# Performance work log

Hardware: AMD Instinct MI355X
Metric: run time of the kernel (lower is better)

The kernel has to match this reference:

```python
import jax, jax.numpy as jnp
import numpy as np

EMBED = 1024
MLP = 2048
N_EXPERTS = 8
TOP_K = 2


def setup_inputs() -> dict:
    key = jax.random.key(0)
    ks = jax.random.split(key, 5)
    scale_e = 1.0 / np.sqrt(EMBED)
    scale_m = 1.0 / np.sqrt(MLP)
    x = jax.random.normal(ks[0], (4, 2048, EMBED), dtype=jnp.float32)
    gate_w = jax.random.normal(ks[1], (EMBED, N_EXPERTS), dtype=jnp.float32) * scale_e
    w1 = jax.random.normal(ks[2], (N_EXPERTS, EMBED, MLP), dtype=jnp.float32) * scale_e
    w3 = jax.random.normal(ks[3], (N_EXPERTS, EMBED, MLP), dtype=jnp.float32) * scale_e
    w2 = jax.random.normal(ks[4], (N_EXPERTS, MLP, EMBED), dtype=jnp.float32) * scale_m
    return {"x": x, "gate_w": gate_w, "w1": w1, "w2": w2, "w3": w3}


def reference(x, gate_w, w1, w2, w3):
    B, S, D = x.shape
    xf = x.reshape(-1, D)  # [T, D] tokens
    # Router: softmax over experts, top-k select, renormalize selected weights
    router_logits = xf @ gate_w                      # [T, E]
    routing_weights = jax.nn.softmax(router_logits, axis=-1)
    sel_w, sel_e = jax.lax.top_k(routing_weights, TOP_K)  # [T, K]
    sel_w = sel_w / jnp.sum(sel_w, axis=-1, keepdims=True)
    out = jnp.zeros_like(xf)
    # Loop over the small fixed expert set; tokens not routed to expert e get
    # coefficient 0, matching the gather/scatter-add combine of the original.
    for e in range(N_EXPERTS):
        coef = jnp.sum(jnp.where(sel_e == e, sel_w, 0.0), axis=-1)  # [T]
        h = jax.nn.silu(xf @ w1[e]) * (xf @ w3[e])                  # [T, Mlp] SwiGLU
        out = out + coef[:, None] * (h @ w2[e])                     # [T, D]
    return out.reshape(B, S, D)
```

## Files before the change

kernel.cpp:

```cpp
#include <hip/hip_runtime.h>

#define EMBED 1024
#define MLP   2048
#define NE    8
#define NTOK  8192
#define RMAX  (2*NTOK + NE*256)

typedef _Float16 f16x8 __attribute__((ext_vector_type(8)));
typedef _Float16 f16x4 __attribute__((ext_vector_type(4)));
typedef float    f32x4 __attribute__((ext_vector_type(4)));

__device__ __forceinline__ void async_copy16(const void* g, void* l) {
  __builtin_amdgcn_global_load_lds(
      (const __attribute__((address_space(1))) unsigned int*)g,
      (__attribute__((address_space(3))) unsigned int*)l, 16, 0, 0);
}

__global__ __launch_bounds__(256) void router_kernel(
    const float* __restrict__ x, const float* __restrict__ gw,
    int* __restrict__ sel_e, float* __restrict__ sel_w, int* __restrict__ counts)
{
  __shared__ float gwt[NE * EMBED];
  __shared__ int cnt[NE];
  int tid = threadIdx.x;
  for (int idx = tid; idx < NE * EMBED; idx += 256) {
    int i = idx >> 3, e = idx & 7;
    gwt[e * EMBED + i] = gw[idx];
  }
  if (tid < NE) cnt[tid] = 0;
  __syncthreads();

  int lane = tid & 63, wv = tid >> 6;
  int t = blockIdx.x * 4 + wv;
  const float4* xr = (const float4*)(x + (size_t)t * EMBED);
  const float4* gt4 = (const float4*)gwt;
  float acc[NE];
  #pragma unroll
  for (int e = 0; e < NE; ++e) acc[e] = 0.f;
  #pragma unroll
  for (int c = 0; c < 4; ++c) {
    float4 xv = xr[c * 64 + lane];
    #pragma unroll
    for (int e = 0; e < NE; ++e) {
      float4 gv = gt4[e * 256 + c * 64 + lane];
      acc[e] += xv.x * gv.x + xv.y * gv.y + xv.z * gv.z + xv.w * gv.w;
    }
  }
  #pragma unroll
  for (int off = 1; off < 64; off <<= 1) {
    #pragma unroll
    for (int e = 0; e < NE; ++e) acc[e] += __shfl_xor(acc[e], off);
  }
  if (lane == 0) {
    int e0 = 0; float l0 = acc[0];
    #pragma unroll
    for (int e = 1; e < NE; ++e) if (acc[e] > l0) { l0 = acc[e]; e0 = e; }
    int e1 = -1; float l1 = -1e30f;
    #pragma unroll
    for (int e = 0; e < NE; ++e) if (e != e0 && acc[e] > l1) { l1 = acc[e]; e1 = e; }
    float w0 = 1.f / (1.f + expf(l1 - l0));
    sel_e[2 * t] = e0;     sel_w[2 * t] = w0;
    sel_e[2 * t + 1] = e1; sel_w[2 * t + 1] = 1.f - w0;
    atomicAdd(&cnt[e0], 1); atomicAdd(&cnt[e1], 1);
  }
  __syncthreads();
  if (tid < NE && cnt[tid]) atomicAdd(&counts[tid], cnt[tid]);
}

__global__ __launch_bounds__(256) void assign_kernel(
    const int* __restrict__ sel_e, const float* __restrict__ sel_w,
    const int* __restrict__ counts, int* __restrict__ cursor,
    int* __restrict__ offs_out, int* __restrict__ rowtok,
    float* __restrict__ rowcoef, int* __restrict__ inv)
{
  int offl[NE];
  {
    int o = 0;
    #pragma unroll
    for (int e = 0; e < NE; ++e) { offl[e] = o; o += (counts[e] + 255) & ~255; }
    if (blockIdx.x == 0 && threadIdx.x == 0) {
      #pragma unroll
      for (int e = 0; e < NE; ++e) offs_out[e] = offl[e];
      offs_out[NE] = o;
    }
  }
  int t = blockIdx.x * 256 + threadIdx.x;
  int lane = threadIdx.x & 63;
  #pragma unroll
  for (int k = 0; k < 2; ++k) {
    int e = sel_e[2 * t + k];
    float w = sel_w[2 * t + k];
    for (int xch = 0; xch < NE; ++xch) {
      unsigned long long m = __ballot(e == xch);
      if (e == xch) {
        int leader = __ffsll((unsigned long long)m) - 1;
        int base = 0;
        if (lane == leader) base = atomicAdd(&cursor[xch], (int)__popcll(m));
        base = __shfl(base, leader);
        int pos = offl[xch] + base + (int)__popcll(m & ((1ull << lane) - 1));
        rowtok[pos] = t;
        rowcoef[pos] = w;
        inv[2 * t + k] = pos;
      }
    }
  }
}

__global__ __launch_bounds__(256) void gather_kernel(
    const float* __restrict__ x, const int* __restrict__ rowtok,
    _Float16* __restrict__ xg)
{
  int r = blockIdx.x;
  int tok = rowtok[r];
  int t4 = threadIdx.x * 4;
  _Float16* dst = xg + (size_t)r * EMBED + t4;
  if (tok >= 0) {
    float4 v = *(const float4*)(x + (size_t)tok * EMBED + t4);
    f16x4 h; h.x = (_Float16)v.x; h.y = (_Float16)v.y; h.z = (_Float16)v.z; h.w = (_Float16)v.w;
    *(f16x4*)dst = h;
  } else {
    f16x4 z = {(_Float16)0.f, (_Float16)0.f, (_Float16)0.f, (_Float16)0.f};
    *(f16x4*)dst = z;
  }
}

__global__ __launch_bounds__(256) void transpose_all_kernel(
    const float* __restrict__ w1, const float* __restrict__ w3,
    const float* __restrict__ w2, _Float16* __restrict__ w1t,
    _Float16* __restrict__ w3t, _Float16* __restrict__ w2t)
{
  int id = blockIdx.x;
  int mat = id >> 12;
  int rr = id & 4095;
  int e = rr >> 9, tile = rr & 511;
  const float* src; _Float16* dst; int K, N;
  if (mat == 0)      { src = w1; dst = w1t; K = EMBED; N = MLP; }
  else if (mat == 1) { src = w3; dst = w3t; K = EMBED; N = MLP; }
  else               { src = w2; dst = w2t; K = MLP;   N = EMBED; }
  int nx = K >> 6;
  int k0 = (tile % nx) * 64, n0 = (tile / nx) * 64;
  src += (size_t)e * K * N;
  dst += (size_t)e * K * N;

  __shared__ float tilebuf[64][65];
  int t = threadIdx.x;
  int r = t >> 4, c4 = (t & 15) * 4;
  #pragma unroll
  for (int i = 0; i < 4; ++i) {
    float4 v = *(const float4*)(src + (size_t)(k0 + r + 16 * i) * N + n0 + c4);
    tilebuf[r + 16 * i][c4 + 0] = v.x;
    tilebuf[r + 16 * i][c4 + 1] = v.y;
    tilebuf[r + 16 * i][c4 + 2] = v.z;
    tilebuf[r + 16 * i][c4 + 3] = v.w;
  }
  __syncthreads();
  int kk8 = (t & 7) * 8, nIdx = t >> 3;
  #pragma unroll
  for (int i = 0; i < 2; ++i) {
    int n = nIdx + 32 * i;
    f16x8 h;
    #pragma unroll
    for (int j = 0; j < 8; ++j) h[j] = (_Float16)tilebuf[kk8 + j][n];
    *(f16x8*)(dst + (size_t)(n0 + n) * K + k0 + kk8) = h;
  }
}

__device__ __forceinline__ int resolve_expert(const int* __restrict__ offs, int r0)
{
  int e = 0;
  #pragma unroll
  for (int q = 0; q < NE - 1; ++q) if (r0 >= offs[q + 1]) e = q + 1;
  return e;
}

__device__ __forceinline__ const _Float16* frag_addr(const _Float16* buf, int row, int quad)
{
  return buf + row * 32 + ((quad ^ ((row >> 1) & 3)) << 3);
}

__global__ __launch_bounds__(512, 2) void gemm1_kernel(
    const _Float16* __restrict__ xg, const _Float16* __restrict__ w1t,
    const _Float16* __restrict__ w3t, const float* __restrict__ rowcoef,
    const int* __restrict__ offs, _Float16* __restrict__ hb)
{
  int r0 = blockIdx.x * 256;
  if (r0 >= offs[NE]) return;
  int e = resolve_expert(offs, r0);
  int n0 = blockIdx.y * 128;
  const _Float16* B1 = w1t + (size_t)e * MLP * EMBED;
  const _Float16* B3 = w3t + (size_t)e * MLP * EMBED;

  __shared__ __align__(16) _Float16 As[2][256 * 32];
  __shared__ __align__(16) _Float16 Bs1[2][128 * 32];
  __shared__ __align__(16) _Float16 Bs3[2][128 * 32];

  int tid = threadIdx.x, lane = tid & 63, wv = tid >> 6;
  int wm = (wv & 3) << 6, wn = (wv >> 2) << 6;
  int l16 = lane & 15, quad = lane >> 4;

  int rowA0 = tid >> 2, kqpA = tid & 3;
  int rowA1 = rowA0 + 128;
  int kqlA0 = kqpA ^ ((rowA0 >> 1) & 3);
  int kqlA1 = kqpA ^ ((rowA1 >> 1) & 3);
  int rowB = tid >> 2, kqpB = tid & 3;
  int kqlB = kqpB ^ ((rowB >> 1) & 3);
  size_t gA0 = (size_t)(r0 + rowA0) * EMBED + kqlA0 * 8;
  size_t gA1 = (size_t)(r0 + rowA1) * EMBED + kqlA1 * 8;
  size_t gB  = (size_t)(n0 + rowB) * EMBED + kqlB * 8;
  int lofA0 = (wv * 64) * 8;
  int lofA1 = (512 + wv * 64) * 8;
  int lofB  = (wv * 64) * 8;

  f32x4 acc1[4][4], acc3[4][4];
  f32x4 z4 = {0.f, 0.f, 0.f, 0.f};
  #pragma unroll
  for (int i = 0; i < 4; ++i)
    #pragma unroll
    for (int j = 0; j < 4; ++j) { acc1[i][j] = z4; acc3[i][j] = z4; }

  auto stage = [&](int b, int kk) {
    async_copy16(xg + gA0 + kk, &As[b][lofA0]);
    async_copy16(xg + gA1 + kk, &As[b][lofA1]);
    async_copy16(B1 + gB  + kk, &Bs1[b][lofB]);
    async_copy16(B3 + gB  + kk, &Bs3[b][lofB]);
  };

  const int NIT = EMBED / 32;
  stage(0, 0);
  for (int k = 0; k < NIT; ++k) {
    int b = k & 1;
    asm volatile("s_waitcnt vmcnt(0)" ::: "memory");
    asm volatile("s_barrier" ::: "memory");
    if (k + 1 < NIT) stage((k + 1) & 1, (k + 1) * 32);

    f16x8 af[4], b1f[4], b3f[4];
    #pragma unroll
    for (int i = 0; i < 4; ++i)
      af[i] = *(const f16x8*)frag_addr(As[b], wm + 16 * i + l16, quad);
    #pragma unroll
    for (int j = 0; j < 4; ++j) {
      b1f[j] = *(const f16x8*)frag_addr(Bs1[b], wn + 16 * j + l16, quad);
      b3f[j] = *(const f16x8*)frag_addr(Bs3[b], wn + 16 * j + l16, quad);
    }
    #pragma unroll
    for (int i = 0; i < 4; ++i)
      #pragma unroll
      for (int j = 0; j < 4; ++j) {
        acc1[i][j] = __builtin_amdgcn_mfma_f32_16x16x32_f16(af[i], b1f[j], acc1[i][j], 0, 0, 0);
        acc3[i][j] = __builtin_amdgcn_mfma_f32_16x16x32_f16(af[i], b3f[j], acc3[i][j], 0, 0, 0);
      }
  }

  #pragma unroll
  for (int i = 0; i < 4; ++i) {
    int mb = r0 + wm + 16 * i + quad * 4;
    float cf[4];
    #pragma unroll
    for (int rg = 0; rg < 4; ++rg) cf[rg] = rowcoef[mb + rg];
    #pragma unroll
    for (int j = 0; j < 4; ++j) {
      int col = n0 + wn + 16 * j + l16;
      #pragma unroll
      for (int rg = 0; rg < 4; ++rg) {
        float g = acc1[i][j][rg], u = acc3[i][j][rg];
        float h = g * u * cf[rg] / (1.f + __expf(-g));
        hb[(size_t)(mb + rg) * MLP + col] = (_Float16)h;
      }
    }
  }
}

__global__ __launch_bounds__(256, 3) void gemm2_kernel(
    const _Float16* __restrict__ hb, const _Float16* __restrict__ w2t,
    const int* __restrict__ offs, _Float16* __restrict__ hb2)
{
  int r0 = blockIdx.x * 128;
  if (r0 >= offs[NE]) return;
  int e = resolve_expert(offs, r0);
  int n0 = blockIdx.y * 128;
  const _Float16* B = w2t + (size_t)e * EMBED * MLP;

  __shared__ __align__(16) _Float16 As[2][128 * 32];
  __shared__ __align__(16) _Float16 Bs[2][128 * 32];

  int tid = threadIdx.x, lane = tid & 63, wv = tid >> 6;
  int wm = (wv & 1) << 6, wn = (wv >> 1) << 6;
  int l16 = lane & 15, quad = lane >> 4;

  int row0 = tid >> 2,         kqp = tid & 3;
  int row1 = (256 + tid) >> 2;
  int kql0 = kqp ^ ((row0 >> 1) & 3);
  int kql1 = kqp ^ ((row1 >> 1) & 3);
  size_t gA0 = (size_t)(r0 + row0) * MLP + kql0 * 8;
  size_t gA1 = (size_t)(r0 + row1) * MLP + kql1 * 8;
  size_t gB0 = (size_t)(n0 + row0) * MLP + kql0 * 8;
  size_t gB1 = (size_t)(n0 + row1) * MLP + kql1 * 8;
  int lof0 = (wv * 64) * 8;
  int lof1 = (256 + wv * 64) * 8;

  f32x4 acc[4][4];
  f32x4 z4 = {0.f, 0.f, 0.f, 0.f};
  #pragma unroll
  for (int i = 0; i < 4; ++i)
    #pragma unroll
    for (int j = 0; j < 4; ++j) acc[i][j] = z4;

  auto stage = [&](int b, int kk) {
    async_copy16(hb + gA0 + kk, &As[b][lof0]);
    async_copy16(hb + gA1 + kk, &As[b][lof1]);
    async_copy16(B  + gB0 + kk, &Bs[b][lof0]);
    async_copy16(B  + gB1 + kk, &Bs[b][lof1]);
  };

  const int NIT = MLP / 32;
  stage(0, 0);
  for (int k = 0; k < NIT; ++k) {
    int b = k & 1;
    asm volatile("s_waitcnt vmcnt(0)" ::: "memory");
    asm volatile("s_barrier" ::: "memory");
    if (k + 1 < NIT) stage((k + 1) & 1, (k + 1) * 32);

    f16x8 af[4], bf[4];
    #pragma unroll
    for (int i = 0; i < 4; ++i)
      af[i] = *(const f16x8*)frag_addr(As[b], wm + 16 * i + l16, quad);
    #pragma unroll
    for (int j = 0; j < 4; ++j)
      bf[j] = *(const f16x8*)frag_addr(Bs[b], wn + 16 * j + l16, quad);
    #pragma unroll
    for (int i = 0; i < 4; ++i)
      #pragma unroll
      for (int j = 0; j < 4; ++j)
        acc[i][j] = __builtin_amdgcn_mfma_f32_16x16x32_f16(af[i], bf[j], acc[i][j], 0, 0, 0);
  }

  #pragma unroll
  for (int i = 0; i < 4; ++i) {
    int mb = r0 + wm + 16 * i + quad * 4;
    #pragma unroll
    for (int j = 0; j < 4; ++j) {
      int col = n0 + wn + 16 * j + l16;
      #pragma unroll
      for (int rg = 0; rg < 4; ++rg)
        hb2[(size_t)(mb + rg) * EMBED + col] = (_Float16)acc[i][j][rg];
    }
  }
}

__global__ __launch_bounds__(256) void combine_kernel(
    const _Float16* __restrict__ hb2, const int* __restrict__ inv,
    float* __restrict__ out)
{
  int t = blockIdx.x;
  int d = threadIdx.x * 4;
  int p0 = inv[2 * t], p1 = inv[2 * t + 1];
  f16x4 a = *(const f16x4*)(hb2 + (size_t)p0 * EMBED + d);
  f16x4 b = *(const f16x4*)(hb2 + (size_t)p1 * EMBED + d);
  float4 r;
  r.x = (float)a.x + (float)b.x;
  r.y = (float)a.y + (float)b.y;
  r.z = (float)a.z + (float)b.z;
  r.w = (float)a.w + (float)b.w;
  *(float4*)(out + (size_t)t * EMBED + d) = r;
}

extern "C" void kernel_launch(void* const* d_in, const int* in_sizes, int n_in,
                              void* d_out, int out_size, void* d_ws, size_t ws_size,
                              hipStream_t stream)
{
  (void)in_sizes; (void)n_in; (void)ws_size; (void)out_size;
  const float* x  = (const float*)d_in[0];
  const float* gw = (const float*)d_in[1];
  const float* w1 = (const float*)d_in[2];
  const float* w2 = (const float*)d_in[3];
  const float* w3 = (const float*)d_in[4];
  float* out = (float*)d_out;
  char* ws = (char*)d_ws;

  size_t o = 0;
  auto alloc = [&](size_t bytes) { size_t r = o; o = (o + bytes + 255) & ~255ULL; return r; };
  const size_t wbytes = (size_t)NE * MLP * EMBED * 2;
  _Float16* w1t = (_Float16*)(ws + alloc(wbytes));
  _Float16* w3t = (_Float16*)(ws + alloc(wbytes));
  _Float16* w2t = (_Float16*)(ws + alloc(wbytes));
  _Float16* xg  = (_Float16*)(ws + alloc((size_t)RMAX * EMBED * 2));
  _Float16* hb  = (_Float16*)(ws + alloc((size_t)RMAX * MLP * 2));
  int*   rowtok  = (int*)(ws + alloc((size_t)RMAX * 4));
  float* rowcoef = (float*)(ws + alloc((size_t)RMAX * 4));
  int*   sel_e   = (int*)(ws + alloc((size_t)2 * NTOK * 4));
  float* sel_w   = (float*)(ws + alloc((size_t)2 * NTOK * 4));
  int*   inv     = (int*)(ws + alloc((size_t)2 * NTOK * 4));
  int*   meta    = (int*)(ws + alloc(256));
  int* counts = meta;
  int* offs   = meta + 8;
  int* cursor = meta + 17;
  _Float16* hb2 = xg;

  hipMemsetAsync(meta, 0, 256, stream);
  hipMemsetAsync(rowtok, 0xFF, (size_t)RMAX * 4, stream);
  hipMemsetAsync(rowcoef, 0, (size_t)RMAX * 4, stream);

  transpose_all_kernel<<<3 * 4096, 256, 0, stream>>>(w1, w3, w2, w1t, w3t, w2t);

  router_kernel<<<NTOK / 4, 256, 0, stream>>>(x, gw, sel_e, sel_w, counts);
  assign_kernel<<<NTOK / 256, 256, 0, stream>>>(sel_e, sel_w, counts, cursor,
                                                offs, rowtok, rowcoef, inv);
  gather_kernel<<<RMAX, 256, 0, stream>>>(x, rowtok, xg);

  gemm1_kernel<<<dim3(RMAX / 256, MLP / 128), 512, 0, stream>>>(xg, w1t, w3t, rowcoef, offs, hb);
  gemm2_kernel<<<dim3(RMAX / 128, EMBED / 128), 256, 0, stream>>>(hb, w2t, offs, hb2);
  combine_kernel<<<NTOK, 256, 0, stream>>>(hb2, inv, out);
}
```

Baseline: 688.4 us.

## Split fused gate/up GEMM into two kernels with shared triple-buffered core

Replaces the fused w1/w3 GEMM (256-row tiles, two accumulators) with two separate 128x128-tile kernels. The first writes the gate result to hb in fp16, and the second reads it back to apply SiLU, the up projection and the routing coefficient. A shared GEMM core macro moves all GEMMs from double to triple buffering, waiting on vmcnt(4) so the next stage's loads overlap compute. Expert padding shrinks from 256 to 128 rows to cut wasted work. In exchange it adds an extra pass over hb, re-reads xg, rounds the gate value to fp16 before SiLU, and adds one more kernel launch.

```diff
diff --git a/kernel.cpp b/kernel.cpp
--- a/kernel.cpp
+++ b/kernel.cpp
@@ -4,7 +4,7 @@
 #define MLP   2048
 #define NE    8
 #define NTOK  8192
-#define RMAX  (2*NTOK + NE*256)
+#define RMAX  (2*NTOK + NE*128)
 
 typedef _Float16 f16x8 __attribute__((ext_vector_type(8)));
 typedef _Float16 f16x4 __attribute__((ext_vector_type(4)));
@@ -77,7 +77,7 @@
   {
     int o = 0;
     #pragma unroll
-    for (int e = 0; e < NE; ++e) { offl[e] = o; o += (counts[e] + 255) & ~255; }
+    for (int e = 0; e < NE; ++e) { offl[e] = o; o += (counts[e] + 127) & ~127; }
     if (blockIdx.x == 0 && threadIdx.x == 0) {
       #pragma unroll
       for (int e = 0; e < NE; ++e) offs_out[e] = offl[e];
@@ -178,79 +178,94 @@
   return buf + row * 32 + ((quad ^ ((row >> 1) & 3)) << 3);
 }
 
-__global__ __launch_bounds__(512, 2) void gemm1_kernel(
+#define GEMM_CORE(Aptr, Bptr, KLEN)                                          \
+  __shared__ __align__(16) _Float16 As[3][128 * 32];                         \
+  __shared__ __align__(16) _Float16 Bs[3][128 * 32];                         \
+  int tid = threadIdx.x, lane = tid & 63, wv = tid >> 6;                     \
+  int wm = (wv & 1) << 6, wn = (wv >> 1) << 6;                               \
+  int l16 = lane & 15, quad = lane >> 4;                                     \
+  int row0 = tid >> 2, kqp = tid & 3;                                        \
+  int row1 = row0 + 64;                                                      \
+  int kql0 = kqp ^ ((row0 >> 1) & 3);                                        \
+  int kql1 = kqp ^ ((row1 >> 1) & 3);                                        \
+  size_t gA0 = (size_t)(r0 + row0) * KLEN + kql0 * 8;                        \
+  size_t gA1 = (size_t)(r0 + row1) * KLEN + kql1 * 8;                        \
+  size_t gB0 = (size_t)(n0 + row0) * KLEN + kql0 * 8;                        \
+  size_t gB1 = (size_t)(n0 + row1) * KLEN + kql1 * 8;                        \
+  int lof0 = (wv * 64) * 8;                                                  \
+  int lof1 = (256 + wv * 64) * 8;                                            \
+  f32x4 acc[4][4];                                                           \
+  f32x4 z4 = {0.f, 0.f, 0.f, 0.f};                                           \
+  _Pragma("unroll")                                                          \
+  for (int i = 0; i < 4; ++i)                                                \
+    _Pragma("unroll")                                                        \
+    for (int j = 0; j < 4; ++j) acc[i][j] = z4;                              \
+  auto stage = [&](int b, int kk) {                                          \
+    async_copy16(Aptr + gA0 + kk, &As[b][lof0]);                             \
+    async_copy16(Aptr + gA1 + kk, &As[b][lof1]);                             \
+    async_copy16(Bptr + gB0 + kk, &Bs[b][lof0]);                             \
+    async_copy16(Bptr + gB1 + kk, &Bs[b][lof1]);                             \
+  };                                                                         \
+  const int NIT = KLEN / 32;                                                 \
+  stage(0, 0);                                                               \
+  for (int k = 0; k < NIT; ++k) {                                            \
+    int b = k % 3;                                                           \
+    if (k + 1 < NIT) {                                                       \
+      stage((k + 1) % 3, (k + 1) * 32);                                      \
+      asm volatile("s_waitcnt vmcnt(4)" ::: "memory");                       \
+    } else {                                                                 \
+      asm volatile("s_waitcnt vmcnt(0)" ::: "memory");                       \
+    }                                                                        \
+    asm volatile("s_barrier" ::: "memory");                                  \
+    f16x8 af[4], bf[4];                                                      \
+    _Pragma("unroll")                                                        \
+    for (int i = 0; i < 4; ++i)                                              \
+      af[i] = *(const f16x8*)frag_addr(As[b], wm + 16 * i + l16, quad);      \
+    _Pragma("unroll")                                                        \
+    for (int j = 0; j < 4; ++j)                                              \
+      bf[j] = *(const f16x8*)frag_addr(Bs[b], wn + 16 * j + l16, quad);      \
+    _Pragma("unroll")                                                        \
+    for (int i = 0; i < 4; ++i)                                              \
+      _Pragma("unroll")                                                      \
+      for (int j = 0; j < 4; ++j)                                            \
+        acc[i][j] = __builtin_amdgcn_mfma_f32_16x16x32_f16(af[i], bf[j],     \
+                                                           acc[i][j], 0,0,0);\
+  }
+
+__global__ __launch_bounds__(256, 3) void gemm1a_kernel(
     const _Float16* __restrict__ xg, const _Float16* __restrict__ w1t,
-    const _Float16* __restrict__ w3t, const float* __restrict__ rowcoef,
     const int* __restrict__ offs, _Float16* __restrict__ hb)
 {
-  int r0 = blockIdx.x * 256;
+  int r0 = blockIdx.x * 128;
   if (r0 >= offs[NE]) return;
   int e = resolve_expert(offs, r0);
   int n0 = blockIdx.y * 128;
   const _Float16* B1 = w1t + (size_t)e * MLP * EMBED;
+  GEMM_CORE(xg, B1, EMBED)
+  #pragma unroll
+  for (int i = 0; i < 4; ++i) {
+    int mb = r0 + wm + 16 * i + quad * 4;
+    #pragma unroll
+    for (int j = 0; j < 4; ++j) {
+      int col = n0 + wn + 16 * j + l16;
+      #pragma unroll
+      for (int rg = 0; rg < 4; ++rg)
+        hb[(size_t)(mb + rg) * MLP + col] = (_Float16)acc[i][j][rg];
+    }
+  }
+}
+
+__global__ __launch_bounds__(256, 3) void gemm1b_kernel(
+    const _Float16* __restrict__ xg, const _Float16* __restrict__ w3t,
+    const float* __restrict__ rowcoef, const int* __restrict__ offs,
+    _Float16* __restrict__ hb)
+{
+  int r0 = blockIdx.x * 128;
+  if (r0 >= offs[NE]) return;
+  int e = resolve_expert(offs, r0);
+  int n0 = blockIdx.y * 128;
   const _Float16* B3 = w3t + (size_t)e * MLP * EMBED;
-
-  __shared__ __align__(16) _Float16 As[2][256 * 32];
-  __shared__ __align__(16) _Float16 Bs1[2][128 * 32];
-  __shared__ __align__(16) _Float16 Bs3[2][128 * 32];
-
-  int tid = threadIdx.x, lane = tid & 63, wv = tid >> 6;
-  int wm = (wv & 3) << 6, wn = (wv >> 2) << 6;
-  int l16 = lane & 15, quad = lane >> 4;
-
-  int rowA0 = tid >> 2, kqpA = tid & 3;
-  int rowA1 = rowA0 + 128;
-  int kqlA0 = kqpA ^ ((rowA0 >> 1) & 3);
-  int kqlA1 = kqpA ^ ((rowA1 >> 1) & 3);
-  int rowB = tid >> 2, kqpB = tid & 3;
-  int kqlB = kqpB ^ ((rowB >> 1) & 3);
-  size_t gA0 = (size_t)(r0 + rowA0) * EMBED + kqlA0 * 8;
-  size_t gA1 = (size_t)(r0 + rowA1) * EMBED + kqlA1 * 8;
-  size_t gB  = (size_t)(n0 + rowB) * EMBED + kqlB * 8;
-  int lofA0 = (wv * 64) * 8;
-  int lofA1 = (512 + wv * 64) * 8;
-  int lofB  = (wv * 64) * 8;
-
-  f32x4 acc1[4][4], acc3[4][4];
-  f32x4 z4 = {0.f, 0.f, 0.f, 0.f};
-  #pragma unroll
-  for (int i = 0; i < 4; ++i)
-    #pragma unroll
-    for (int j = 0; j < 4; ++j) { acc1[i][j] = z4; acc3[i][j] = z4; }
-
-  auto stage = [&](int b, int kk) {
-    async_copy16(xg + gA0 + kk, &As[b][lofA0]);
-    async_copy16(xg + gA1 + kk, &As[b][lofA1]);
-    async_copy16(B1 + gB  + kk, &Bs1[b][lofB]);
-    async_copy16(B3 + gB  + kk, &Bs3[b][lofB]);
-  };
-
-  const int NIT = EMBED / 32;
-  stage(0, 0);
-  for (int k = 0; k < NIT; ++k) {
-    int b = k & 1;
-    asm volatile("s_waitcnt vmcnt(0)" ::: "memory");
-    asm volatile("s_barrier" ::: "memory");
-    if (k + 1 < NIT) stage((k + 1) & 1, (k + 1) * 32);
-
-    f16x8 af[4], b1f[4], b3f[4];
-    #pragma unroll
-    for (int i = 0; i < 4; ++i)
-      af[i] = *(const f16x8*)frag_addr(As[b], wm + 16 * i + l16, quad);
-    #pragma unroll
-    for (int j = 0; j < 4; ++j) {
-      b1f[j] = *(const f16x8*)frag_addr(Bs1[b], wn + 16 * j + l16, quad);
-      b3f[j] = *(const f16x8*)frag_addr(Bs3[b], wn + 16 * j + l16, quad);
-    }
-    #pragma unroll
-    for (int i = 0; i < 4; ++i)
-      #pragma unroll
-      for (int j = 0; j < 4; ++j) {
-        acc1[i][j] = __builtin_amdgcn_mfma_f32_16x16x32_f16(af[i], b1f[j], acc1[i][j], 0, 0, 0);
-        acc3[i][j] = __builtin_amdgcn_mfma_f32_16x16x32_f16(af[i], b3f[j], acc3[i][j], 0, 0, 0);
-      }
-  }
-
+  GEMM_CORE(xg, B3, EMBED)
   #pragma unroll
   for (int i = 0; i < 4; ++i) {
     int mb = r0 + wm + 16 * i + quad * 4;
@@ -262,7 +277,8 @@
       int col = n0 + wn + 16 * j + l16;
       #pragma unroll
       for (int rg = 0; rg < 4; ++rg) {
-        float g = acc1[i][j][rg], u = acc3[i][j][rg];
+        float g = (float)hb[(size_t)(mb + rg) * MLP + col];
+        float u = acc[i][j][rg];
         float h = g * u * cf[rg] / (1.f + __expf(-g));
         hb[(size_t)(mb + rg) * MLP + col] = (_Float16)h;
       }
@@ -279,61 +295,7 @@
   int e = resolve_expert(offs, r0);
   int n0 = blockIdx.y * 128;
   const _Float16* B = w2t + (size_t)e * EMBED * MLP;
-
-  __shared__ __align__(16) _Float16 As[2][128 * 32];
-  __shared__ __align__(16) _Float16 Bs[2][128 * 32];
-
-  int tid = threadIdx.x, lane = tid & 63, wv = tid >> 6;
-  int wm = (wv & 1) << 6, wn = (wv >> 1) << 6;
-  int l16 = lane & 15, quad = lane >> 4;
-
-  int row0 = tid >> 2,         kqp = tid & 3;
-  int row1 = (256 + tid) >> 2;
-  int kql0 = kqp ^ ((row0 >> 1) & 3);
-  int kql1 = kqp ^ ((row1 >> 1) & 3);
-  size_t gA0 = (size_t)(r0 + row0) * MLP + kql0 * 8;
-  size_t gA1 = (size_t)(r0 + row1) * MLP + kql1 * 8;
-  size_t gB0 = (size_t)(n0 + row0) * MLP + kql0 * 8;
-  size_t gB1 = (size_t)(n0 + row1) * MLP + kql1 * 8;
-  int lof0 = (wv * 64) * 8;
-  int lof1 = (256 + wv * 64) * 8;
-
-  f32x4 acc[4][4];
-  f32x4 z4 = {0.f, 0.f, 0.f, 0.f};
-  #pragma unroll
-  for (int i = 0; i < 4; ++i)
-    #pragma unroll
-    for (int j = 0; j < 4; ++j) acc[i][j] = z4;
-
-  auto stage = [&](int b, int kk) {
-    async_copy16(hb + gA0 + kk, &As[b][lof0]);
-    async_copy16(hb + gA1 + kk, &As[b][lof1]);
-    async_copy16(B  + gB0 + kk, &Bs[b][lof0]);
-    async_copy16(B  + gB1 + kk, &Bs[b][lof1]);
-  };
-
-  const int NIT = MLP / 32;
-  stage(0, 0);
-  for (int k = 0; k < NIT; ++k) {
-    int b = k & 1;
-    asm volatile("s_waitcnt vmcnt(0)" ::: "memory");
-    asm volatile("s_barrier" ::: "memory");
-    if (k + 1 < NIT) stage((k + 1) & 1, (k + 1) * 32);
-
-    f16x8 af[4], bf[4];
-    #pragma unroll
-    for (int i = 0; i < 4; ++i)
-      af[i] = *(const f16x8*)frag_addr(As[b], wm + 16 * i + l16, quad);
-    #pragma unroll
-    for (int j = 0; j < 4; ++j)
-      bf[j] = *(const f16x8*)frag_addr(Bs[b], wn + 16 * j + l16, quad);
-    #pragma unroll
-    for (int i = 0; i < 4; ++i)
-      #pragma unroll
-      for (int j = 0; j < 4; ++j)
-        acc[i][j] = __builtin_amdgcn_mfma_f32_16x16x32_f16(af[i], bf[j], acc[i][j], 0, 0, 0);
-  }
-
+  GEMM_CORE(hb, B, MLP)
   #pragma unroll
   for (int i = 0; i < 4; ++i) {
     int mb = r0 + wm + 16 * i + quad * 4;
@@ -407,7 +369,8 @@
                                                 offs, rowtok, rowcoef, inv);
   gather_kernel<<<RMAX, 256, 0, stream>>>(x, rowtok, xg);
 
-  gemm1_kernel<<<dim3(RMAX / 256, MLP / 128), 512, 0, stream>>>(xg, w1t, w3t, rowcoef, offs, hb);
+  gemm1a_kernel<<<dim3(RMAX / 128, MLP / 128), 256, 0, stream>>>(xg, w1t, offs, hb);
+  gemm1b_kernel<<<dim3(RMAX / 128, MLP / 128), 256, 0, stream>>>(xg, w3t, rowcoef, offs, hb);
   gemm2_kernel<<<dim3(RMAX / 128, EMBED / 128), 256, 0, stream>>>(hb, w2t, offs, hb2);
   combine_kernel<<<NTOK, 256, 0, stream>>>(hb2, inv, out);
 }
```

After: 674.3 us. 1.02x faster.
